# Performance work log

Hardware: AMD Instinct MI355X
Metric: run time of the kernel (lower is better)

Reference implementation:

```python
import jax, jax.numpy as jnp
import numpy as np

N, C, H, W = 32, 1, 512, 1024
SAMPLE_NUM = 5000
SIGMA = 0.03
ALPHA = 1.0
EPS = 1e-6
LOSS_WEIGHT = 1.0


def setup_inputs() -> dict:
    key = jax.random.key(0)
    k0, k1, k2, k3 = jax.random.split(key, 4)
    prediction = jax.random.normal(k0, (N, C, H, W), dtype=jnp.float32)
    # depths strictly > 0 so target > mask_value (=-1e-8) holds for every pixel,
    # matching the common case where all pixels are 'effective'.
    target = jax.random.uniform(k1, (N, C, H, W), dtype=jnp.float32,
                                minval=0.1, maxval=10.0)
    mask = jax.random.randint(k2, (N, C, H, W), 0, 2).astype(bool)
    # per-image random permutation of pixel indices -> disjoint pairs (A, B),
    # reproducing torch.randperm-based pair sampling as constant indices.
    perm = jax.vmap(lambda k: jax.random.permutation(k, H * W))(
        jax.random.split(k3, N))                      # [N, H*W] int32
    idx_A = perm[:, 0:2 * SAMPLE_NUM:2]               # [N, S]
    idx_B = perm[:, 1:2 * SAMPLE_NUM:2]               # [N, S]
    return {"prediction": prediction, "target": target, "mask": mask,
            "idx_A": idx_A, "idx_B": idx_B}


def reference(prediction, target, mask, idx_A, idx_B):
    n = target.shape[0]
    p = prediction.reshape(n, -1)   # [N, H*W]
    t = target.reshape(n, -1)
    m = mask.reshape(n, -1)

    iA = jnp.take_along_axis(p, idx_A, axis=1)   # [N, S]
    iB = jnp.take_along_axis(p, idx_B, axis=1)
    tA = jnp.take_along_axis(t, idx_A, axis=1)
    tB = jnp.take_along_axis(t, idx_B, axis=1)
    mA = jnp.take_along_axis(m, idx_A, axis=1)
    mB = jnpp_take(m, idx_B) if False else jnp.take_along_axis(m, idx_B, axis=1)

    ratio = tA / (tB + EPS)
    hi = 1.0 + SIGMA
    lo = 1.0 / (1.0 + SIGMA)
    mask_eq = (ratio < hi) & (ratio > lo)
    labels = jnp.where(ratio >= hi, 1.0,
                       jnp.where(ratio <= lo, -1.0, 0.0)).astype(p.dtype)
    cmask = mA & mB

    eq_sel = mask_eq & cmask
    uneq_sel = (~mask_eq) & cmask

    equal_loss = jnp.where(eq_sel, (iA - iB) ** 2, 0.0).sum()
    unequal_loss = jnp.where(
        uneq_sel, jnp.log1p(jnp.exp((iB - iA) * labels)), 0.0).sum()
    valid_samples = cmask.sum().astype(p.dtype)

    loss = (ALPHA * equal_loss + unequal_loss) / (valid_samples + EPS)
    return loss * LOSS_WEIGHT
```

## Files before the change

### kernel.cpp

```cpp
#include <hip/hip_runtime.h>
#include <math.h>

#define SAMPLE_NUM 5000
#define HWSZ (512 * 1024)
#define SIGMA_F 0.03f
#define EPS_F 1e-6f
#define BLOCK 256
#define NTOT 32
#define PACK_WORDS64 (NTOT * HWSZ / 64)
#define ROW_BITS_PAD 5120
#define BM_OFF_BYTES 8192
#define PK_OFF_BYTES 32768
#define VBLK_PER_ROW 8
#define PAIRS_PER_VBLK 640


__device__ __forceinline__ unsigned pack16_bytes(uint4 v) {
  const unsigned n0 = ((v.x & 0x01010101u) * 0x01020408u) >> 24;
  const unsigned n1 = ((v.y & 0x01010101u) * 0x01020408u) >> 24;
  const unsigned n2 = ((v.z & 0x01010101u) * 0x01020408u) >> 24;
  const unsigned n3 = ((v.w & 0x01010101u) * 0x01020408u) >> 24;
  return (n0 & 0xFu) | ((n1 & 0xFu) << 4) | ((n2 & 0xFu) << 8) |
         ((n3 & 0xFu) << 12);
}

__device__ __forceinline__ unsigned lsb4_i32(uint4 v) {
  return (v.x & 1u) | ((v.y & 1u) << 1) | ((v.z & 1u) << 2) |
         ((v.w & 1u) << 3);
}

__global__ void __launch_bounds__(BLOCK)
mask_pack(const void* __restrict__ mask_raw,
          unsigned long long* __restrict__ out) {
  const unsigned int* mw = (const unsigned int*)mask_raw;
  bool mask_is_i32 = true;
  #pragma unroll
  for (int w = 0; w < 32; ++w) {
    if (mw[w] > 1u) mask_is_i32 = false;
  }

  const int i = blockIdx.x * BLOCK + threadIdx.x;
  if (i >= PACK_WORDS64) return;

  unsigned long long r;
  if (!mask_is_i32) {
    const uint4* src = (const uint4*)mask_raw + (i * 4);
    const uint4 v0 = src[0];
    const uint4 v1 = src[1];
    const uint4 v2 = src[2];
    const uint4 v3 = src[3];
    r = (unsigned long long)pack16_bytes(v0) |
        ((unsigned long long)pack16_bytes(v1) << 16) |
        ((unsigned long long)pack16_bytes(v2) << 32) |
        ((unsigned long long)pack16_bytes(v3) << 48);
  } else {
    const uint4* src = (const uint4*)mask_raw + (i * 16);
    unsigned long long acc = 0ull;
    #pragma unroll
    for (int k = 0; k < 16; ++k) {
      acc |= (unsigned long long)lsb4_i32(src[k]) << (4 * k);
    }
    r = acc;
  }
  out[i] = r;
}

__global__ void __launch_bounds__(1024)
mask_validity(const unsigned int* __restrict__ mpack32,
              const int* __restrict__ idxA, const int* __restrict__ idxB,
              unsigned long long* __restrict__ bitmap) {
  extern __shared__ unsigned int sbm[];
  const int bid = blockIdx.x;
  const int n = bid >> 3;
  const int sub = bid & 7;
  const int t = threadIdx.x;

  const uint4* src = (const uint4*)(mpack32 + n * (HWSZ / 32));
  uint4* dst = (uint4*)sbm;
  #pragma unroll
  for (int it = 0; it < 4; ++it) {
    dst[t + it * 1024] = src[t + it * 1024];
  }
  __syncthreads();

  const int lane = t & 63;
  const int wv = t >> 6;
  if (wv < 10) {
    const int il = sub * PAIRS_PER_VBLK + wv * 64 + lane;
    bool valid = false;
    if (il < SAMPLE_NUM) {
      const int i = n * SAMPLE_NUM + il;
      const int a = idxA[i];
      const int b = idxB[i];
      valid =
          ((sbm[a >> 5] >> (a & 31)) & (sbm[b >> 5] >> (b & 31)) & 1u) != 0u;
    }
    const unsigned long long bal = __ballot(valid);
    if (lane == 0) {
      bitmap[n * (ROW_BITS_PAD / 64) + sub * 10 + wv] = bal;
    }
  }
}

__global__ void __launch_bounds__(BLOCK)
ranking_loss_partial(const float* __restrict__ pred,
                     const float* __restrict__ targ,
                     const unsigned int* __restrict__ bitmap32,
                     const int* __restrict__ idxA,
                     const int* __restrict__ idxB,
                     float* __restrict__ ws, int total) {
  const float hi = 1.0f + SIGMA_F;
  const float lo = 1.0f / (1.0f + SIGMA_F);

  float eq_sum = 0.0f, uneq_sum = 0.0f, valid = 0.0f;
  const int i = blockIdx.x * BLOCK + threadIdx.x;
  if (i < total) {
    const int n = i / SAMPLE_NUM;
    const int il = i - n * SAMPLE_NUM;
    const unsigned w = bitmap32[n * (ROW_BITS_PAD / 32) + (il >> 5)];
    const int a = idxA[i];
    const int b = idxB[i];

    if ((w >> (il & 31)) & 1u) {
      const int base = n * HWSZ;
      const int ia_off = base + a;
      const int ib_off = base + b;
      const float tA = targ[ia_off];
      const float tB = targ[ib_off];
      const float iA = pred[ia_off];
      const float iB = pred[ib_off];

      valid = 1.0f;
      const float ratio = tA / (tB + EPS_F);
      if (ratio < hi && ratio > lo) {
        const float d = iA - iB;
        eq_sum = d * d;
      } else {
        const float label = (ratio >= hi) ? 1.0f : -1.0f;
        const float x = (iB - iA) * label;
        uneq_sum = (x > 20.0f) ? x : log1pf(expf(x));
      }
    }
  }

  #pragma unroll
  for (int off = 32; off > 0; off >>= 1) {
    eq_sum   += __shfl_down(eq_sum, off, 64);
    uneq_sum += __shfl_down(uneq_sum, off, 64);
    valid    += __shfl_down(valid, off, 64);
  }

  __shared__ float s_eq[4], s_un[4], s_va[4];
  const int lane = threadIdx.x & 63;
  const int wave = threadIdx.x >> 6;
  if (lane == 0) {
    s_eq[wave] = eq_sum;
    s_un[wave] = uneq_sum;
    s_va[wave] = valid;
  }
  __syncthreads();

  if (threadIdx.x == 0) {
    float e = 0.0f, u = 0.0f, v = 0.0f;
    #pragma unroll
    for (int w2 = 0; w2 < BLOCK / 64; ++w2) {
      e += s_eq[w2];
      u += s_un[w2];
      v += s_va[w2];
    }
    float* slot = ws + 3 * blockIdx.x;
    slot[0] = e;
    slot[1] = u;
    slot[2] = v;
  }
}

__global__ void __launch_bounds__(BLOCK)
ranking_loss_finalize(const float* __restrict__ ws, float* __restrict__ out,
                      int nblocks) {
  float e = 0.0f, u = 0.0f, v = 0.0f;
  for (int s = threadIdx.x; s < nblocks; s += BLOCK) {
    e += ws[3 * s + 0];
    u += ws[3 * s + 1];
    v += ws[3 * s + 2];
  }
  #pragma unroll
  for (int off = 32; off > 0; off >>= 1) {
    e += __shfl_down(e, off, 64);
    u += __shfl_down(u, off, 64);
    v += __shfl_down(v, off, 64);
  }
  __shared__ float s_e[4], s_u[4], s_v[4];
  const int lane = threadIdx.x & 63;
  const int wave = threadIdx.x >> 6;
  if (lane == 0) {
    s_e[wave] = e;
    s_u[wave] = u;
    s_v[wave] = v;
  }
  __syncthreads();
  if (threadIdx.x == 0) {
    float te = 0.0f, tu = 0.0f, tv = 0.0f;
    #pragma unroll
    for (int w = 0; w < BLOCK / 64; ++w) {
      te += s_e[w];
      tu += s_u[w];
      tv += s_v[w];
    }
    out[0] = (te + tu) / (tv + EPS_F);
  }
}

extern "C" void kernel_launch(void* const* d_in, const int* in_sizes, int n_in,
                              void* d_out, int out_size, void* d_ws,
                              size_t ws_size, hipStream_t stream) {
  const float* pred = (const float*)d_in[0];
  const float* targ = (const float*)d_in[1];
  const void* mask = d_in[2];
  const int* idxA = (const int*)d_in[3];
  const int* idxB = (const int*)d_in[4];
  float* out = (float*)d_out;
  float* ws = (float*)d_ws;

  const int total = in_sizes[3];
  const int rows = total / SAMPLE_NUM;
  const int grid = (total + BLOCK - 1) / BLOCK;

  unsigned long long* mpack64 =
      (unsigned long long*)((char*)d_ws + PK_OFF_BYTES);
  const unsigned int* mpack32 = (const unsigned int*)mpack64;
  unsigned long long* bm64 =
      (unsigned long long*)((char*)d_ws + BM_OFF_BYTES);
  const unsigned int* bm32 = (const unsigned int*)bm64;

  mask_pack<<<PACK_WORDS64 / BLOCK, BLOCK, 0, stream>>>(mask, mpack64);
  mask_validity<<<rows * VBLK_PER_ROW, 1024, HWSZ / 8, stream>>>(
      mpack32, idxA, idxB, bm64);
  ranking_loss_partial<<<grid, BLOCK, 0, stream>>>(pred, targ, bm32, idxA,
                                                   idxB, ws, total);
  ranking_loss_finalize<<<1, BLOCK, 0, stream>>>(ws, out, grid);
}
```

Before: 184.1 us.

## Fuse mask packing, validity, loss and finalize into one cooperative kernel

Replaces the four separate launches (mask pack, validity bitmap, partial loss, finalize) with one cooperative kernel that uses grid-wide syncs between phases. Validity is now tested directly against the shared-memory packed mask, so the intermediate ballot bitmap round-trip disappears, and the partial sums are reduced by block 0 after a second grid sync. This removes launch overhead and the intermediate global traffic. In exchange the mask pack runs on only 256 blocks of 1024 threads with a grid-stride loop and needs cooperative-launch co-residency, which the 64KB of shared memory per block may limit.

Result: slower. 260.0 us (+41.2%).

```diff
diff --git a/kernel.cpp b/kernel.cpp
--- a/kernel.cpp
+++ b/kernel.cpp
@@ -1,19 +1,18 @@
 #include <hip/hip_runtime.h>
+#include <hip/hip_cooperative_groups.h>
 #include <math.h>
 
 #define SAMPLE_NUM 5000
 #define HWSZ (512 * 1024)
 #define SIGMA_F 0.03f
 #define EPS_F 1e-6f
-#define BLOCK 256
-#define NTOT 32
-#define PACK_WORDS64 (NTOT * HWSZ / 64)
-#define ROW_BITS_PAD 5120
-#define BM_OFF_BYTES 8192
-#define PK_OFF_BYTES 32768
+#define THREADS 1024
 #define VBLK_PER_ROW 8
 #define PAIRS_PER_VBLK 640
-
+#define PK_OFF_BYTES 32768
+
+
+namespace cg = cooperative_groups;
 
 __device__ __forceinline__ unsigned pack16_bytes(uint4 v) {
   const unsigned n0 = ((v.x & 0x01010101u) * 0x01020408u) >> 24;
@@ -29,9 +28,22 @@
          ((v.w & 1u) << 3);
 }
 
-__global__ void __launch_bounds__(BLOCK)
-mask_pack(const void* __restrict__ mask_raw,
-          unsigned long long* __restrict__ out) {
+__global__ void __launch_bounds__(THREADS)
+ranking_loss_fused(const float* __restrict__ pred,
+                   const float* __restrict__ targ,
+                   const void* __restrict__ mask_raw,
+                   const int* __restrict__ idxA,
+                   const int* __restrict__ idxB,
+                   unsigned long long* __restrict__ mpack64,
+                   float* __restrict__ slots, float* __restrict__ out,
+                   int total) {
+  __shared__ unsigned int sbm[HWSZ / 32];
+  const int t = threadIdx.x;
+  const int bid = blockIdx.x;
+  const int nblocks = gridDim.x;
+  const int rows = total / SAMPLE_NUM;
+  const int words64 = rows * (HWSZ / 64);
+
   const unsigned int* mw = (const unsigned int*)mask_raw;
   bool mask_is_i32 = true;
   #pragma unroll
@@ -39,89 +51,56 @@
     if (mw[w] > 1u) mask_is_i32 = false;
   }
 
-  const int i = blockIdx.x * BLOCK + threadIdx.x;
-  if (i >= PACK_WORDS64) return;
-
-  unsigned long long r;
-  if (!mask_is_i32) {
-    const uint4* src = (const uint4*)mask_raw + (i * 4);
-    const uint4 v0 = src[0];
-    const uint4 v1 = src[1];
-    const uint4 v2 = src[2];
-    const uint4 v3 = src[3];
-    r = (unsigned long long)pack16_bytes(v0) |
-        ((unsigned long long)pack16_bytes(v1) << 16) |
-        ((unsigned long long)pack16_bytes(v2) << 32) |
-        ((unsigned long long)pack16_bytes(v3) << 48);
-  } else {
-    const uint4* src = (const uint4*)mask_raw + (i * 16);
-    unsigned long long acc = 0ull;
-    #pragma unroll
-    for (int k = 0; k < 16; ++k) {
-      acc |= (unsigned long long)lsb4_i32(src[k]) << (4 * k);
-    }
-    r = acc;
-  }
-  out[i] = r;
-}
-
-__global__ void __launch_bounds__(1024)
-mask_validity(const unsigned int* __restrict__ mpack32,
-              const int* __restrict__ idxA, const int* __restrict__ idxB,
-              unsigned long long* __restrict__ bitmap) {
-  extern __shared__ unsigned int sbm[];
-  const int bid = blockIdx.x;
+  for (int i = bid * THREADS + t; i < words64; i += nblocks * THREADS) {
+    unsigned long long r;
+    if (!mask_is_i32) {
+      const uint4* src = (const uint4*)mask_raw + (i * 4);
+      const uint4 v0 = src[0];
+      const uint4 v1 = src[1];
+      const uint4 v2 = src[2];
+      const uint4 v3 = src[3];
+      r = (unsigned long long)pack16_bytes(v0) |
+          ((unsigned long long)pack16_bytes(v1) << 16) |
+          ((unsigned long long)pack16_bytes(v2) << 32) |
+          ((unsigned long long)pack16_bytes(v3) << 48);
+    } else {
+      const uint4* src = (const uint4*)mask_raw + (i * 16);
+      unsigned long long acc = 0ull;
+      #pragma unroll
+      for (int k = 0; k < 16; ++k) {
+        acc |= (unsigned long long)lsb4_i32(src[k]) << (4 * k);
+      }
+      r = acc;
+    }
+    mpack64[i] = r;
+  }
+
+  cg::this_grid().sync();
+
   const int n = bid >> 3;
   const int sub = bid & 7;
-  const int t = threadIdx.x;
-
-  const uint4* src = (const uint4*)(mpack32 + n * (HWSZ / 32));
-  uint4* dst = (uint4*)sbm;
-  #pragma unroll
-  for (int it = 0; it < 4; ++it) {
-    dst[t + it * 1024] = src[t + it * 1024];
+  {
+    const uint4* src =
+        (const uint4*)((const unsigned int*)mpack64 + n * (HWSZ / 32));
+    uint4* dst = (uint4*)sbm;
+    #pragma unroll
+    for (int it = 0; it < 4; ++it) {
+      dst[t + it * THREADS] = src[t + it * THREADS];
+    }
   }
   __syncthreads();
 
+  const float hi = 1.0f + SIGMA_F;
+  const float lo = 1.0f / (1.0f + SIGMA_F);
+  float eq_sum = 0.0f, uneq_sum = 0.0f, valid = 0.0f;
   const int lane = t & 63;
   const int wv = t >> 6;
-  if (wv < 10) {
-    const int il = sub * PAIRS_PER_VBLK + wv * 64 + lane;
-    bool valid = false;
-    if (il < SAMPLE_NUM) {
-      const int i = n * SAMPLE_NUM + il;
-      const int a = idxA[i];
-      const int b = idxB[i];
-      valid =
-          ((sbm[a >> 5] >> (a & 31)) & (sbm[b >> 5] >> (b & 31)) & 1u) != 0u;
-    }
-    const unsigned long long bal = __ballot(valid);
-    if (lane == 0) {
-      bitmap[n * (ROW_BITS_PAD / 64) + sub * 10 + wv] = bal;
-    }
-  }
-}
-
-__global__ void __launch_bounds__(BLOCK)
-ranking_loss_partial(const float* __restrict__ pred,
-                     const float* __restrict__ targ,
-                     const unsigned int* __restrict__ bitmap32,
-                     const int* __restrict__ idxA,
-                     const int* __restrict__ idxB,
-                     float* __restrict__ ws, int total) {
-  const float hi = 1.0f + SIGMA_F;
-  const float lo = 1.0f / (1.0f + SIGMA_F);
-
-  float eq_sum = 0.0f, uneq_sum = 0.0f, valid = 0.0f;
-  const int i = blockIdx.x * BLOCK + threadIdx.x;
-  if (i < total) {
-    const int n = i / SAMPLE_NUM;
-    const int il = i - n * SAMPLE_NUM;
-    const unsigned w = bitmap32[n * (ROW_BITS_PAD / 32) + (il >> 5)];
+  const int il = sub * PAIRS_PER_VBLK + wv * 64 + lane;
+  if (wv < 10 && il < SAMPLE_NUM) {
+    const int i = n * SAMPLE_NUM + il;
     const int a = idxA[i];
     const int b = idxB[i];
-
-    if ((w >> (il & 31)) & 1u) {
+    if ((sbm[a >> 5] >> (a & 31)) & (sbm[b >> 5] >> (b & 31)) & 1u) {
       const int base = n * HWSZ;
       const int ia_off = base + a;
       const int ib_off = base + b;
@@ -150,64 +129,60 @@
     valid    += __shfl_down(valid, off, 64);
   }
 
-  __shared__ float s_eq[4], s_un[4], s_va[4];
-  const int lane = threadIdx.x & 63;
-  const int wave = threadIdx.x >> 6;
+  __syncthreads();
+  float* sf = (float*)sbm;
   if (lane == 0) {
-    s_eq[wave] = eq_sum;
-    s_un[wave] = uneq_sum;
-    s_va[wave] = valid;
+    sf[wv * 3 + 0] = eq_sum;
+    sf[wv * 3 + 1] = uneq_sum;
+    sf[wv * 3 + 2] = valid;
   }
   __syncthreads();
-
-  if (threadIdx.x == 0) {
+  if (t == 0) {
     float e = 0.0f, u = 0.0f, v = 0.0f;
     #pragma unroll
-    for (int w2 = 0; w2 < BLOCK / 64; ++w2) {
-      e += s_eq[w2];
-      u += s_un[w2];
-      v += s_va[w2];
-    }
-    float* slot = ws + 3 * blockIdx.x;
+    for (int w = 0; w < THREADS / 64; ++w) {
+      e += sf[w * 3 + 0];
+      u += sf[w * 3 + 1];
+      v += sf[w * 3 + 2];
+    }
+    float* slot = slots + 3 * bid;
     slot[0] = e;
     slot[1] = u;
     slot[2] = v;
   }
-}
-
-__global__ void __launch_bounds__(BLOCK)
-ranking_loss_finalize(const float* __restrict__ ws, float* __restrict__ out,
-                      int nblocks) {
-  float e = 0.0f, u = 0.0f, v = 0.0f;
-  for (int s = threadIdx.x; s < nblocks; s += BLOCK) {
-    e += ws[3 * s + 0];
-    u += ws[3 * s + 1];
-    v += ws[3 * s + 2];
-  }
-  #pragma unroll
-  for (int off = 32; off > 0; off >>= 1) {
-    e += __shfl_down(e, off, 64);
-    u += __shfl_down(u, off, 64);
-    v += __shfl_down(v, off, 64);
-  }
-  __shared__ float s_e[4], s_u[4], s_v[4];
-  const int lane = threadIdx.x & 63;
-  const int wave = threadIdx.x >> 6;
-  if (lane == 0) {
-    s_e[wave] = e;
-    s_u[wave] = u;
-    s_v[wave] = v;
-  }
-  __syncthreads();
-  if (threadIdx.x == 0) {
-    float te = 0.0f, tu = 0.0f, tv = 0.0f;
+
+  cg::this_grid().sync();
+
+  if (bid == 0) {
+    float e = 0.0f, u = 0.0f, v = 0.0f;
+    for (int s = t; s < nblocks; s += THREADS) {
+      e += slots[3 * s + 0];
+      u += slots[3 * s + 1];
+      v += slots[3 * s + 2];
+    }
     #pragma unroll
-    for (int w = 0; w < BLOCK / 64; ++w) {
-      te += s_e[w];
-      tu += s_u[w];
-      tv += s_v[w];
-    }
-    out[0] = (te + tu) / (tv + EPS_F);
+    for (int off = 32; off > 0; off >>= 1) {
+      e += __shfl_down(e, off, 64);
+      u += __shfl_down(u, off, 64);
+      v += __shfl_down(v, off, 64);
+    }
+    __syncthreads();
+    if (lane == 0) {
+      sf[wv * 3 + 0] = e;
+      sf[wv * 3 + 1] = u;
+      sf[wv * 3 + 2] = v;
+    }
+    __syncthreads();
+    if (t == 0) {
+      float te = 0.0f, tu = 0.0f, tv = 0.0f;
+      #pragma unroll
+      for (int w = 0; w < THREADS / 64; ++w) {
+        te += sf[w * 3 + 0];
+        tu += sf[w * 3 + 1];
+        tv += sf[w * 3 + 2];
+      }
+      out[0] = (te + tu) / (tv + EPS_F);
+    }
   }
 }
 
@@ -220,23 +195,18 @@
   const int* idxA = (const int*)d_in[3];
   const int* idxB = (const int*)d_in[4];
   float* out = (float*)d_out;
-  float* ws = (float*)d_ws;
-
-  const int total = in_sizes[3];
-  const int rows = total / SAMPLE_NUM;
-  const int grid = (total + BLOCK - 1) / BLOCK;
-
+  float* slots = (float*)d_ws;
   unsigned long long* mpack64 =
       (unsigned long long*)((char*)d_ws + PK_OFF_BYTES);
-  const unsigned int* mpack32 = (const unsigned int*)mpack64;
-  unsigned long long* bm64 =
-      (unsigned long long*)((char*)d_ws + BM_OFF_BYTES);
-  const unsigned int* bm32 = (const unsigned int*)bm64;
-
-  mask_pack<<<PACK_WORDS64 / BLOCK, BLOCK, 0, stream>>>(mask, mpack64);
-  mask_validity<<<rows * VBLK_PER_ROW, 1024, HWSZ / 8, stream>>>(
-      mpack32, idxA, idxB, bm64);
-  ranking_loss_partial<<<grid, BLOCK, 0, stream>>>(pred, targ, bm32, idxA,
-                                                   idxB, ws, total);
-  ranking_loss_finalize<<<1, BLOCK, 0, stream>>>(ws, out, grid);
-}
+
+  int total = in_sizes[3];
+  const int rows = total / SAMPLE_NUM;
+
+  void* args[] = {(void*)&pred, (void*)&targ,  (void*)&mask,
+                  (void*)&idxA, (void*)&idxB,  (void*)&mpack64,
+                  (void*)&slots, (void*)&out,  (void*)&total};
+  dim3 grid(rows * VBLK_PER_ROW);
+  dim3 block(THREADS);
+  hipLaunchCooperativeKernel((const void*)ranking_loss_fused, grid, block,
+                             args, 0, stream);
+}
```
